# Kernel tuning notes

Measured on AMD Instinct MI355X. Metric: run time of the kernel, lower is better.

The kernel has to match this reference:

```python
import jax, jax.numpy as jnp
import numpy as np

N_HEADS = 4
NEG_SLOPE = 0.2  # DGL GATConv default leaky_relu slope


def setup_inputs() -> dict:
    key = jax.random.key(0)
    ks = jax.random.split(key, 12)
    N, E = 50000, 800000
    in_dim, time_dim, out_dim = 128, 128, 128
    d_head = out_dim // N_HEADS
    in_total = in_dim + time_dim
    h = jax.random.normal(ks[0], (N, in_dim), jnp.float32)
    time_tensor = jax.random.uniform(ks[1], (E,), jnp.float32)
    src = jax.random.randint(ks[2], (E,), 0, N, jnp.int32)
    dst = jax.random.randint(ks[3], (E,), 0, N, jnp.int32)
    # TimeEncoding: Linear(1, time_dim) with xavier weight, zero bias
    w_t = jax.random.normal(ks[4], (time_dim, 1), jnp.float32) * (6.0 / (1 + time_dim)) ** 0.5
    b_t = jnp.zeros((time_dim,), jnp.float32)
    # GATConv params
    W_fc = jax.random.normal(ks[5], (N_HEADS * d_head, in_total), jnp.float32) * (2.0 / in_total) ** 0.5
    attn_l = jax.random.normal(ks[6], (N_HEADS, d_head), jnp.float32) * 0.1
    attn_r = jax.random.normal(ks[7], (N_HEADS, d_head), jnp.float32) * 0.1
    W_res = jax.random.normal(ks[8], (N_HEADS * d_head, in_total), jnp.float32) * (2.0 / in_total) ** 0.5
    bias = jnp.zeros((N_HEADS * d_head,), jnp.float32)
    return {"h": h, "time_tensor": time_tensor, "src": src, "dst": dst,
            "num_nodes": N, "w_t": w_t, "b_t": b_t, "W_fc": W_fc,
            "attn_l": attn_l, "attn_r": attn_r, "W_res": W_res, "bias": bias}


def reference(h, time_tensor, src, dst, num_nodes, w_t, b_t, W_fc, attn_l, attn_r, W_res, bias):
    N = num_nodes
    E = src.shape[0]
    # Time encoding: cos(W t + b), per edge -> [E, time_dim]
    time_emb = jnp.cos(time_tensor[:, None] * w_t[:, 0][None, :] + b_t[None, :])
    # Mailbox mean of concat([src h, time_emb]) per dst node.
    # mean(concat) == concat(mean, mean), so sum the two halves separately.
    ones = jnp.ones((E,), h.dtype)
    deg = jax.ops.segment_sum(ones, dst, num_segments=N)  # [N]
    sum_h = jax.ops.segment_sum(h[src], dst, num_segments=N)       # [N, in_dim]
    sum_t = jax.ops.segment_sum(time_emb, dst, num_segments=N)     # [N, time_dim]
    inv_deg = 1.0 / jnp.maximum(deg, 1.0)
    h_time = jnp.concatenate([sum_h, sum_t], axis=1) * inv_deg[:, None]  # [N, in+time]
    # GATConv (eval mode, no dropout)
    d_head = W_fc.shape[0] // N_HEADS
    feat = (h_time @ W_fc.T).reshape(N, N_HEADS, d_head)  # [N,H,D]
    el = jnp.sum(feat * attn_l[None], axis=-1)  # [N,H]
    er = jnp.sum(feat * attn_r[None], axis=-1)  # [N,H]
    e = el[src] + er[dst]                        # [E,H]
    e = jnp.where(e > 0, e, NEG_SLOPE * e)
    # edge softmax over incoming edges of each dst node
    m = jax.ops.segment_max(e, dst, num_segments=N)  # [N,H]
    m = jnp.where(jnp.isfinite(m), m, 0.0)
    ex = jnp.exp(e - m[dst])
    denom = jax.ops.segment_sum(ex, dst, num_segments=N)
    a = ex / jnp.maximum(denom[dst], 1e-9)           # [E,H]
    rst = jax.ops.segment_sum(a[:, :, None] * feat[src], dst, num_segments=N)  # [N,H,D]
    res = (h_time @ W_res.T).reshape(N, N_HEADS, d_head)
    out = rst + res + bias.reshape(1, N_HEADS, d_head)
    out = jax.nn.elu(out)
    return out.reshape(N, -1)  # [N, out_dim]
```

## Files before the change

kernel.cpp:

```cpp
#include <hip/hip_runtime.h>
#include <math.h>

#define NH 4
#define NEG_SLOPE 0.2f
#define BKT_SHIFT 8
#define EPB 4096
#define CBLK 8192
#define INV2PI 0.15915494309189535f
#define LOG2E  1.4426950408889634f

typedef __attribute__((ext_vector_type(8))) short bf16x8;
typedef __attribute__((ext_vector_type(4))) float f32x4;
typedef __attribute__((ext_vector_type(2))) float f32x2;

__device__ __forceinline__ float blo(unsigned u) { return __uint_as_float(u << 16); }
__device__ __forceinline__ float bhi(unsigned u) { return __uint_as_float(u & 0xFFFF0000u); }
__device__ __forceinline__ f32x2 mk2(float a, float b) { f32x2 r; r.x = a; r.y = b; return r; }
__device__ __forceinline__ f32x2 unpk(unsigned u) { return mk2(blo(u), bhi(u)); }
__device__ __forceinline__ unsigned short rne(float f) {
    unsigned u = __float_as_uint(f);
    u += 0x7FFFu + ((u >> 16) & 1u);
    return (unsigned short)(u >> 16);
}
__device__ __forceinline__ unsigned pack2(float a, float b) {
    return (unsigned)rne(a) | ((unsigned)rne(b) << 16);
}

__global__ __launch_bounds__(256) void k_prep(
    const float* __restrict__ h, unsigned* __restrict__ hbu, int n_pairs,
    const float* __restrict__ Wfc, const float* __restrict__ Wres,
    unsigned* __restrict__ wcat,
    const float* __restrict__ w_t, const float* __restrict__ b_t,
    float2* __restrict__ w_s, float2* __restrict__ b_s,
    const int* __restrict__ dst, int* __restrict__ bkt_cnt, int E, int NB, int EB) {
    __shared__ int cnt[256];
    int tid = threadIdx.x;
    int t = blockIdx.x * blockDim.x + tid;
    if (t < n_pairs) {
        float2 v = ((const float2*)h)[t];
        hbu[t] = pack2(v.x, v.y);
    }
    if (t < 32768) {
        int col = t >> 7, kk = t & 127;
        const float* srcp = (col < 128) ? (Wfc + (size_t)col * 256)
                                        : (Wres + (size_t)(col - 128) * 256);
        float2 v = ((const float2*)srcp)[kk];
        int s  = col >> 6, ct = (col >> 4) & 3, r = col & 15;
        int ks = kk >> 4,  q  = (kk >> 2) & 3,  d = kk & 3;
        int w2i = ((s * 32 + ks * 4 + ct) << 8) + ((q * 16 + r) << 2) + d;
        wcat[w2i] = pack2(v.x, v.y);
    }
    if (t < 64) {
        float2 wv = ((const float2*)w_t)[t];
        float2 bv = ((const float2*)b_t)[t];
        w_s[t] = make_float2(wv.x * INV2PI, wv.y * INV2PI);
        b_s[t] = make_float2(bv.x * INV2PI, bv.y * INV2PI);
    }
    if (blockIdx.x < (unsigned)EB) {
        cnt[tid] = 0;
        __syncthreads();
        int q0 = (blockIdx.x * CBLK) >> 2;
#pragma unroll
        for (int k = 0; k < CBLK / 1024; k++) {
            int qi = q0 + k * 256 + tid;
            int base = qi * 4;
            if (base + 3 < E) {
                int4 dd = ((const int4*)dst)[qi];
                atomicAdd(&cnt[dd.x >> BKT_SHIFT], 1);
                atomicAdd(&cnt[dd.y >> BKT_SHIFT], 1);
                atomicAdd(&cnt[dd.z >> BKT_SHIFT], 1);
                atomicAdd(&cnt[dd.w >> BKT_SHIFT], 1);
            } else {
                for (int e = base; e < E; e++) atomicAdd(&cnt[dst[e] >> BKT_SHIFT], 1);
            }
        }
        __syncthreads();
        if (tid < NB) {
            int c = cnt[tid];
            if (c) atomicAdd(bkt_cnt + tid, c);
        }
    }
}

__global__ __launch_bounds__(256) void k_bktscan(
    const int* __restrict__ bkt_cnt, int* __restrict__ bkt_start,
    int* __restrict__ bkt_cursor, int* __restrict__ row_start,
    int NB, int E, int N) {
    __shared__ int wsum[4];
    int tid = threadIdx.x, lane = tid & 63, wid = tid >> 6;
    int v = (tid < NB) ? bkt_cnt[tid] : 0;
    int x = v;
#pragma unroll
    for (int off = 1; off < 64; off <<= 1) {
        int y = __shfl_up(x, off, 64);
        if (lane >= off) x += y;
    }
    if (lane == 63) wsum[wid] = x;
    __syncthreads();
    if (tid == 0) {
        int s = 0;
#pragma unroll
        for (int k = 0; k < 4; k++) { int tk = wsum[k]; wsum[k] = s; s += tk; }
    }
    __syncthreads();
    int excl = wsum[wid] + x - v;
    if (tid < NB) { bkt_start[tid] = excl; bkt_cursor[tid] = excl; }
    if (tid == 0) { bkt_start[NB] = E; row_start[N] = E; }
}

__global__ __launch_bounds__(256) void k_binscatter(
    const int* __restrict__ src, const int* __restrict__ dst,
    const float* __restrict__ tt, int* __restrict__ bkt_cursor,
    uint2* __restrict__ staged, int E, int NB) {
    __shared__ int cnt[1024];
    __shared__ int basep[1024];
    int e0 = blockIdx.x * EPB;
    int tid = threadIdx.x;
    for (int b = tid; b < NB; b += 256) cnt[b] = 0;
    __syncthreads();
#pragma unroll
    for (int k = 0; k < EPB / 256; k++) {
        int e = e0 + k * 256 + tid;
        if (e < E) atomicAdd(&cnt[dst[e] >> BKT_SHIFT], 1);
    }
    __syncthreads();
    for (int b = tid; b < NB; b += 256) {
        int c = cnt[b];
        basep[b] = (c > 0) ? atomicAdd(bkt_cursor + b, c) : 0;
        cnt[b] = 0;
    }
    __syncthreads();
#pragma unroll
    for (int k = 0; k < EPB / 256; k++) {
        int e = e0 + k * 256 + tid;
        if (e < E) {
            int d = dst[e];
            int b = d >> BKT_SHIFT;
            int r = atomicAdd(&cnt[b], 1);
            unsigned tq = min((unsigned)(tt[e] * 32768.0f), 32767u);
            staged[basep[b] + r] =
                make_uint2(((unsigned)src[e] << 15) | tq, (unsigned)(d & 255));
        }
    }
}

__global__ __launch_bounds__(256) void k_binsort(
    const uint2* __restrict__ staged, const int* __restrict__ bkt_start,
    int* __restrict__ row_start, unsigned* __restrict__ est, int N) {
    __shared__ int cnt[256];
    __shared__ int cur[256];
    __shared__ int wsum[4];
    __shared__ uint2 sst[8192];
    int b = blockIdx.x;
    int n0 = b << BKT_SHIFT;
    int tid = threadIdx.x;
    cnt[tid] = 0;
    __syncthreads();
    int s0 = bkt_start[b], s1 = bkt_start[b + 1];
    int run = s1 - s0;
    for (int p = tid; p < run; p += 256) {
        uint2 v = staged[s0 + p];
        if (p < 8192) sst[p] = v;
        atomicAdd(&cnt[v.y], 1);
    }
    __syncthreads();
    int lane = tid & 63, wid = tid >> 6;
    int v = cnt[tid];
    int x = v;
#pragma unroll
    for (int off = 1; off < 64; off <<= 1) {
        int y = __shfl_up(x, off, 64);
        if (lane >= off) x += y;
    }
    if (lane == 63) wsum[wid] = x;
    __syncthreads();
    if (tid == 0) {
        int s = 0;
#pragma unroll
        for (int k = 0; k < 4; k++) { int tk = wsum[k]; wsum[k] = s; s += tk; }
    }
    __syncthreads();
    int excl = s0 + wsum[wid] + x - v;
    cur[tid] = excl;
    if (n0 + tid < N) row_start[n0 + tid] = excl;
    __syncthreads();
    for (int p = tid; p < run; p += 256) {
        uint2 vv = (p < 8192) ? sst[p] : staged[s0 + p];
        int pos = atomicAdd(&cur[vv.y], 1);
        est[pos] = vv.x;
    }
}

__device__ __forceinline__ void agg_edge(unsigned u, const char* __restrict__ hb,
                                         int i, const f32x2* wv, const f32x2* bv,
                                         f32x2* aH, f32x2* aT) {
    unsigned off = (u >> 15) << 8;
    float t = (float)(u & 0x7FFFu) * (1.0f / 32768.0f) + (0.5f / 32768.0f);
    uint4 hv = *(const uint4*)(hb + off + i * 16);
    aH[0] += unpk(hv.x);
    aH[1] += unpk(hv.y);
    aH[2] += unpk(hv.z);
    aH[3] += unpk(hv.w);
    f32x2 t2 = mk2(t, t);
    f32x2 a0 = t2 * wv[0] + bv[0];
    f32x2 a1 = t2 * wv[1] + bv[1];
    f32x2 a2 = t2 * wv[2] + bv[2];
    f32x2 a3 = t2 * wv[3] + bv[3];
    aT[0] += mk2(__builtin_amdgcn_cosf(a0.x), __builtin_amdgcn_cosf(a0.y));
    aT[1] += mk2(__builtin_amdgcn_cosf(a1.x), __builtin_amdgcn_cosf(a1.y));
    aT[2] += mk2(__builtin_amdgcn_cosf(a2.x), __builtin_amdgcn_cosf(a2.y));
    aT[3] += mk2(__builtin_amdgcn_cosf(a3.x), __builtin_amdgcn_cosf(a3.y));
}

__device__ __forceinline__ void attn_edge(unsigned u, const char* __restrict__ fb,
                                          int i, int hd, const char* __restrict__ elb,
                                          float erh, f32x2* acc, float& den) {
    unsigned off = (u >> 15) << 8;
    float elh = *(const float*)(elb + (off >> 4) + (hd << 2));
    uint4 fv = *(const uint4*)(fb + off + i * 16);
    float w = elh + erh; w = w > 0.f ? w : NEG_SLOPE * w;
    float ex = __builtin_amdgcn_exp2f(w);
    f32x2 ex2 = mk2(ex, ex);
    acc[0] = ex2 * unpk(fv.x) + acc[0];
    acc[1] = ex2 * unpk(fv.y) + acc[1];
    acc[2] = ex2 * unpk(fv.z) + acc[2];
    acc[3] = ex2 * unpk(fv.w) + acc[3];
    den += ex;
}

__global__ __launch_bounds__(256) void k_agg(
    const unsigned* __restrict__ hbu, const unsigned* __restrict__ est,
    const int* __restrict__ row_start,
    const float2* __restrict__ w_s, const float2* __restrict__ b_s,
    unsigned* __restrict__ htu, int N) {
    int n = blockIdx.x * 4 + (threadIdx.x >> 6);
    if (n >= N) return;
    int lane = threadIdx.x & 63;
    int g = lane >> 4, i = lane & 15;
    int rs = row_start[n], re = row_start[n + 1];
    const char* hb = (const char*)hbu;
    const f32x2* wp = (const f32x2*)w_s;
    const f32x2* bp = (const f32x2*)b_s;
    f32x2 wv[4], bv[4];
#pragma unroll
    for (int k = 0; k < 4; k++) { wv[k] = wp[4 * i + k]; bv[k] = bp[4 * i + k]; }
    f32x2 aH[4] = {}, aT[4] = {};
    int nb = (re - rs) >> 4;
    int e = rs + g;
    for (int j = 0; j < nb; j++, e += 16) {
        unsigned u0 = est[e];
        unsigned u1 = est[e + 4];
        unsigned u2 = est[e + 8];
        unsigned u3 = est[e + 12];
        agg_edge(u0, hb, i, wv, bv, aH, aT);
        agg_edge(u1, hb, i, wv, bv, aH, aT);
        agg_edge(u2, hb, i, wv, bv, aH, aT);
        agg_edge(u3, hb, i, wv, bv, aH, aT);
    }
    for (; e < re; e += 4)
        agg_edge(est[e], hb, i, wv, bv, aH, aT);
#pragma unroll
    for (int off = 16; off <= 32; off <<= 1) {
#pragma unroll
        for (int k = 0; k < 4; k++) {
            aH[k].x += __shfl_xor(aH[k].x, off, 64);
            aH[k].y += __shfl_xor(aH[k].y, off, 64);
            aT[k].x += __shfl_xor(aT[k].x, off, 64);
            aT[k].y += __shfl_xor(aT[k].y, off, 64);
        }
    }
    if (g == 0) {
        int deg = re - rs;
        float idg = (deg > 0) ? 1.0f / (float)deg : 1.0f;
        uint4* ht4 = (uint4*)htu;
        uint4 oh, ot;
        oh.x = pack2(aH[0].x * idg, aH[0].y * idg);
        oh.y = pack2(aH[1].x * idg, aH[1].y * idg);
        oh.z = pack2(aH[2].x * idg, aH[2].y * idg);
        oh.w = pack2(aH[3].x * idg, aH[3].y * idg);
        ot.x = pack2(aT[0].x * idg, aT[0].y * idg);
        ot.y = pack2(aT[1].x * idg, aT[1].y * idg);
        ot.z = pack2(aT[2].x * idg, aT[2].y * idg);
        ot.w = pack2(aT[3].x * idg, aT[3].y * idg);
        ht4[(size_t)n * 32 + i]      = oh;
        ht4[(size_t)n * 32 + 16 + i] = ot;
    }
}

__global__ __launch_bounds__(256) void k_gemm(
    const unsigned short* __restrict__ ht, const unsigned* __restrict__ wcat,
    unsigned short* __restrict__ feat, float* __restrict__ res_out, int N) {
    __shared__ __align__(16) unsigned short As[64 * 264];
    int tid = threadIdx.x;
    int row0 = blockIdx.x * 64;
    const uint4* src4 = (const uint4*)ht;
    for (int idx = tid; idx < 64 * 32; idx += 256) {
        int rl = idx >> 5, c16 = idx & 31;
        int gr = row0 + rl; if (gr >= N) gr = N - 1;
        uint4 v = src4[(size_t)gr * 32 + c16];
        *(uint4*)(As + rl * 264 + c16 * 8) = v;
    }
    __syncthreads();
    int wave = tid >> 6, lane = tid & 63;
    int r = lane & 15, q = lane >> 4;
    int colbase = wave * 64;
    const bf16x8* bbase = (const bf16x8*)wcat + (size_t)wave * 2048 + lane;
    const unsigned short* abase = As + r * 264 + q * 8;
    f32x4 acc[4][4] = {};
#pragma unroll
    for (int ks = 0; ks < 8; ks++) {
        bf16x8 a[4], b[4];
#pragma unroll
        for (int rt = 0; rt < 4; rt++)
            a[rt] = *(const bf16x8*)(abase + rt * (16 * 264) + ks * 32);
#pragma unroll
        for (int ct = 0; ct < 4; ct++)
            b[ct] = bbase[(ks * 4 + ct) * 64];
#pragma unroll
        for (int rt = 0; rt < 4; rt++)
#pragma unroll
            for (int ct = 0; ct < 4; ct++)
                acc[rt][ct] = __builtin_amdgcn_mfma_f32_16x16x32_bf16(a[rt], b[ct], acc[rt][ct], 0, 0, 0);
    }
    bool featw = (colbase < 128);
#pragma unroll
    for (int rt = 0; rt < 4; rt++) {
        int rb = row0 + rt * 16 + q * 4;
#pragma unroll
        for (int ct = 0; ct < 4; ct++) {
            int col = colbase + ct * 16 + r;
#pragma unroll
            for (int reg = 0; reg < 4; reg++) {
                int row = rb + reg;
                if (row >= N) continue;
                float v = acc[rt][ct][reg];
                if (featw) feat[(size_t)row * 128 + col] = rne(v);
                else       res_out[(size_t)row * 128 + (col - 128)] = v;
            }
        }
    }
}

__global__ void k_el_er(const unsigned* __restrict__ featu,
                        const float* __restrict__ attn_l, const float* __restrict__ attn_r,
                        float* __restrict__ el, float* __restrict__ er, int NH4) {
    int t = blockIdx.x * blockDim.x + threadIdx.x;
    if (t >= NH4) return;
    int n = t >> 2, hd = t & 3;
    const unsigned* f = featu + (size_t)n * 64 + hd * 16;
    const float2* al = (const float2*)(attn_l + hd * 32);
    const float2* ar = (const float2*)(attn_r + hd * 32);
    float sl = 0.f, sr = 0.f;
#pragma unroll
    for (int i = 0; i < 16; i++) {
        unsigned u = f[i];
        float f0 = blo(u), f1 = bhi(u);
        float2 a = al[i], b = ar[i];
        sl = fmaf(f0, a.x, fmaf(f1, a.y, sl));
        sr = fmaf(f0, b.x, fmaf(f1, b.y, sr));
    }
    el[t] = sl * LOG2E;
    er[t] = sr * LOG2E;
}

__global__ __launch_bounds__(256) void k_attn(
    const unsigned* __restrict__ est, const int* __restrict__ row_start,
    const float* __restrict__ el, const float* __restrict__ er,
    const unsigned* __restrict__ featu, const float* __restrict__ bias,
    float* __restrict__ out, int N) {
    int n = blockIdx.x * 4 + (threadIdx.x >> 6);
    if (n >= N) return;
    int lane = threadIdx.x & 63;
    int g = lane >> 4, i = lane & 15;
    int hd = i >> 2;
    int rs = row_start[n], re = row_start[n + 1];
    float erh = er[(size_t)n * 4 + hd];
    const char* fb = (const char*)featu;
    const char* elb = (const char*)el;
    f32x2 acc[4] = {};
    float den = 0.f;
    int nb = (re - rs) >> 4;
    int e = rs + g;
    for (int j = 0; j < nb; j++, e += 16) {
        unsigned u0 = est[e];
        unsigned u1 = est[e + 4];
        unsigned u2 = est[e + 8];
        unsigned u3 = est[e + 12];
        attn_edge(u0, fb, i, hd, elb, erh, acc, den);
        attn_edge(u1, fb, i, hd, elb, erh, acc, den);
        attn_edge(u2, fb, i, hd, elb, erh, acc, den);
        attn_edge(u3, fb, i, hd, elb, erh, acc, den);
    }
    for (; e < re; e += 4)
        attn_edge(est[e], fb, i, hd, elb, erh, acc, den);
#pragma unroll
    for (int off = 16; off <= 32; off <<= 1) {
#pragma unroll
        for (int k = 0; k < 4; k++) {
            acc[k].x += __shfl_xor(acc[k].x, off, 64);
            acc[k].y += __shfl_xor(acc[k].y, off, 64);
        }
        den += __shfl_xor(den, off, 64);
    }
    if (g == 0) {
        float id = 1.0f / fmaxf(den, 1e-9f);
        float* op = out + (size_t)n * 128 + i * 8;
        const float* bp = bias + i * 8;
        float4 o0 = ((const float4*)op)[0], o1 = ((const float4*)op)[1];
        float4 b0 = ((const float4*)bp)[0], b1 = ((const float4*)bp)[1];
        float4 r0, r1;
        r0.x = fmaf(acc[0].x, id, o0.x + b0.x);
        r0.y = fmaf(acc[0].y, id, o0.y + b0.y);
        r0.z = fmaf(acc[1].x, id, o0.z + b0.z);
        r0.w = fmaf(acc[1].y, id, o0.w + b0.w);
        r1.x = fmaf(acc[2].x, id, o1.x + b1.x);
        r1.y = fmaf(acc[2].y, id, o1.y + b1.y);
        r1.z = fmaf(acc[3].x, id, o1.z + b1.z);
        r1.w = fmaf(acc[3].y, id, o1.w + b1.w);
        r0.x = r0.x > 0.f ? r0.x : (__expf(r0.x) - 1.0f);
        r0.y = r0.y > 0.f ? r0.y : (__expf(r0.y) - 1.0f);
        r0.z = r0.z > 0.f ? r0.z : (__expf(r0.z) - 1.0f);
        r0.w = r0.w > 0.f ? r0.w : (__expf(r0.w) - 1.0f);
        r1.x = r1.x > 0.f ? r1.x : (__expf(r1.x) - 1.0f);
        r1.y = r1.y > 0.f ? r1.y : (__expf(r1.y) - 1.0f);
        r1.z = r1.z > 0.f ? r1.z : (__expf(r1.z) - 1.0f);
        r1.w = r1.w > 0.f ? r1.w : (__expf(r1.w) - 1.0f);
        ((float4*)op)[0] = r0;
        ((float4*)op)[1] = r1;
    }
}

extern "C" void kernel_launch(void* const* d_in, const int* in_sizes, int n_in,
                              void* d_out, int out_size, void* d_ws, size_t ws_size,
                              hipStream_t stream) {
    const float* h     = (const float*)d_in[0];
    const float* tt    = (const float*)d_in[1];
    const int*   src   = (const int*)d_in[2];
    const int*   dst   = (const int*)d_in[3];
    const float* w_t   = (const float*)d_in[5];
    const float* b_t   = (const float*)d_in[6];
    const float* W_fc  = (const float*)d_in[7];
    const float* al    = (const float*)d_in[8];
    const float* ar    = (const float*)d_in[9];
    const float* W_res = (const float*)d_in[10];
    const float* bias  = (const float*)d_in[11];

    int N = in_sizes[0] / 128;
    int E = in_sizes[1];
    int NB = (N + 255) >> BKT_SHIFT;
    int EB = (E + CBLK - 1) / CBLK;

    char* ws = (char*)d_ws;
    size_t off = 0;
    auto alloc = [&](size_t bytes) { void* p = ws + off; off = (off + bytes + 15) & ~(size_t)15; return p; };
    unsigned* htu     = (unsigned*)alloc((size_t)N * 128 * 4);
    unsigned* hbu     = (unsigned*)alloc((size_t)N * 64 * 4);
    unsigned* featu   = (unsigned*)alloc((size_t)N * 64 * 4);
    unsigned* wcat    = (unsigned*)alloc(32768 * 4);
    float2*   w_s     = (float2*)alloc(64 * 8);
    float2*   b_s     = (float2*)alloc(64 * 8);
    float*    el      = (float*)alloc((size_t)N * NH * 4);
    float*    er      = (float*)alloc((size_t)N * NH * 4);
    int*      row_st  = (int*)alloc((size_t)(N + 1) * 4);
    int*      bkt_cur = (int*)alloc((size_t)NB * 4);
    int*      bkt_cnt = (int*)alloc((size_t)NB * 4);
    int*      bkt_sta = (int*)alloc((size_t)(NB + 1) * 4);
    unsigned* est     = (unsigned*)alloc((size_t)E * 4);
    uint2*    staged  = (uint2*)featu;

    hipMemsetAsync(bkt_cnt, 0, (size_t)NB * 4, stream);

    int prep_n = N * 64;
    hipLaunchKernelGGL(k_prep, dim3((prep_n + 255) / 256), dim3(256), 0, stream,
                       h, hbu, prep_n, W_fc, W_res, wcat, w_t, b_t, w_s, b_s,
                       dst, bkt_cnt, E, NB, EB);
    hipLaunchKernelGGL(k_bktscan, dim3(1), dim3(256), 0, stream,
                       bkt_cnt, bkt_sta, bkt_cur, row_st, NB, E, N);
    hipLaunchKernelGGL(k_binscatter, dim3((E + EPB - 1) / EPB), dim3(256), 0, stream,
                       src, dst, tt, bkt_cur, staged, E, NB);
    hipLaunchKernelGGL(k_binsort, dim3(NB), dim3(256), 0, stream,
                       staged, bkt_sta, row_st, est, N);
    hipLaunchKernelGGL(k_agg, dim3((N + 3) / 4), dim3(256), 0, stream,
                       hbu, est, row_st, w_s, b_s, htu, N);
    hipLaunchKernelGGL(k_gemm, dim3((N + 63) / 64), dim3(256), 0, stream,
                       (const unsigned short*)htu, wcat,
                       (unsigned short*)featu, (float*)d_out, N);
    hipLaunchKernelGGL(k_el_er, dim3((N * NH + 255) / 256), dim3(256), 0, stream,
                       featu, al, ar, el, er, N * NH);
    hipLaunchKernelGGL(k_attn, dim3((N + 3) / 4), dim3(256), 0, stream,
                       est, row_st, el, er, featu, bias, (float*)d_out, N);
}
```

Baseline: 249.0 us.

## Use precomputed cosine table for time encoding and persistent grid-stride agg/attn kernels

Replaces per-edge cosine evaluation in the aggregation kernel with a lookup into a 4096x128 cosine table built in k_prep, with the quantized time index truncated to 12 bits. Makes k_agg and k_attn persistent grid-stride kernels capped at 2048 blocks. Removes the shared-memory staging buffer in k_binsort so it reads staged entries from global memory twice. The table trades transcendental work for extra memory traffic and coarser time quantization, and the persistent loop may hurt load balance.

```diff
diff --git a/kernel.cpp b/kernel.cpp
--- a/kernel.cpp
+++ b/kernel.cpp
@@ -6,6 +6,7 @@
 #define BKT_SHIFT 8
 #define EPB 4096
 #define CBLK 8192
+#define TBLK 2048
 #define INV2PI 0.15915494309189535f
 #define LOG2E  1.4426950408889634f
 
@@ -31,7 +32,7 @@
     const float* __restrict__ Wfc, const float* __restrict__ Wres,
     unsigned* __restrict__ wcat,
     const float* __restrict__ w_t, const float* __restrict__ b_t,
-    float2* __restrict__ w_s, float2* __restrict__ b_s,
+    float* __restrict__ tbl,
     const int* __restrict__ dst, int* __restrict__ bkt_cnt, int E, int NB, int EB) {
     __shared__ int cnt[256];
     int tid = threadIdx.x;
@@ -49,12 +50,6 @@
         int ks = kk >> 4,  q  = (kk >> 2) & 3,  d = kk & 3;
         int w2i = ((s * 32 + ks * 4 + ct) << 8) + ((q * 16 + r) << 2) + d;
         wcat[w2i] = pack2(v.x, v.y);
-    }
-    if (t < 64) {
-        float2 wv = ((const float2*)w_t)[t];
-        float2 bv = ((const float2*)b_t)[t];
-        w_s[t] = make_float2(wv.x * INV2PI, wv.y * INV2PI);
-        b_s[t] = make_float2(bv.x * INV2PI, bv.y * INV2PI);
     }
     if (blockIdx.x < (unsigned)EB) {
         cnt[tid] = 0;
@@ -80,6 +75,15 @@
             if (c) atomicAdd(bkt_cnt + tid, c);
         }
     }
+    int tb = blockIdx.x - EB;
+    if (tb >= 0 && tb < TBLK) {
+        int idx = tb * 256 + tid;
+        int j = idx >> 7, d = idx & 127;
+        float wv = w_t[d] * INV2PI;
+        float bv = b_t[d] * INV2PI;
+        float tv = ((float)j + 0.5f) * (1.0f / 4096.0f);
+        tbl[idx] = __builtin_amdgcn_cosf(fmaf(tv, wv, bv));
+    }
 }
 
 __global__ __launch_bounds__(256) void k_bktscan(
@@ -150,19 +154,14 @@
     __shared__ int cnt[256];
     __shared__ int cur[256];
     __shared__ int wsum[4];
-    __shared__ uint2 sst[8192];
     int b = blockIdx.x;
     int n0 = b << BKT_SHIFT;
     int tid = threadIdx.x;
     cnt[tid] = 0;
     __syncthreads();
     int s0 = bkt_start[b], s1 = bkt_start[b + 1];
-    int run = s1 - s0;
-    for (int p = tid; p < run; p += 256) {
-        uint2 v = staged[s0 + p];
-        if (p < 8192) sst[p] = v;
-        atomicAdd(&cnt[v.y], 1);
-    }
+    for (int p = s0 + tid; p < s1; p += 256)
+        atomicAdd(&cnt[staged[p].y], 1);
     __syncthreads();
     int lane = tid & 63, wid = tid >> 6;
     int v = cnt[tid];
@@ -184,32 +183,29 @@
     cur[tid] = excl;
     if (n0 + tid < N) row_start[n0 + tid] = excl;
     __syncthreads();
-    for (int p = tid; p < run; p += 256) {
-        uint2 vv = (p < 8192) ? sst[p] : staged[s0 + p];
+    for (int p = s0 + tid; p < s1; p += 256) {
+        uint2 vv = staged[p];
         int pos = atomicAdd(&cur[vv.y], 1);
         est[pos] = vv.x;
     }
 }
 
 __device__ __forceinline__ void agg_edge(unsigned u, const char* __restrict__ hb,
-                                         int i, const f32x2* wv, const f32x2* bv,
+                                         const char* __restrict__ tb, int i,
                                          f32x2* aH, f32x2* aT) {
-    unsigned off = (u >> 15) << 8;
-    float t = (float)(u & 0x7FFFu) * (1.0f / 32768.0f) + (0.5f / 32768.0f);
-    uint4 hv = *(const uint4*)(hb + off + i * 16);
+    unsigned hoff = (u >> 15) << 8;
+    unsigned toff = (u & 0x7FF8u) << 6;
+    uint4 hv = *(const uint4*)(hb + hoff + i * 16);
+    const f32x4* cp = (const f32x4*)(tb + toff + i * 32);
+    f32x4 c0 = cp[0], c1 = cp[1];
     aH[0] += unpk(hv.x);
     aH[1] += unpk(hv.y);
     aH[2] += unpk(hv.z);
     aH[3] += unpk(hv.w);
-    f32x2 t2 = mk2(t, t);
-    f32x2 a0 = t2 * wv[0] + bv[0];
-    f32x2 a1 = t2 * wv[1] + bv[1];
-    f32x2 a2 = t2 * wv[2] + bv[2];
-    f32x2 a3 = t2 * wv[3] + bv[3];
-    aT[0] += mk2(__builtin_amdgcn_cosf(a0.x), __builtin_amdgcn_cosf(a0.y));
-    aT[1] += mk2(__builtin_amdgcn_cosf(a1.x), __builtin_amdgcn_cosf(a1.y));
-    aT[2] += mk2(__builtin_amdgcn_cosf(a2.x), __builtin_amdgcn_cosf(a2.y));
-    aT[3] += mk2(__builtin_amdgcn_cosf(a3.x), __builtin_amdgcn_cosf(a3.y));
+    aT[0] += mk2(c0.x, c0.y);
+    aT[1] += mk2(c0.z, c0.w);
+    aT[2] += mk2(c1.x, c1.y);
+    aT[3] += mk2(c1.z, c1.w);
 }
 
 __device__ __forceinline__ void attn_edge(unsigned u, const char* __restrict__ fb,
@@ -229,61 +225,58 @@
 }
 
 __global__ __launch_bounds__(256) void k_agg(
-    const unsigned* __restrict__ hbu, const unsigned* __restrict__ est,
-    const int* __restrict__ row_start,
-    const float2* __restrict__ w_s, const float2* __restrict__ b_s,
+    const unsigned* __restrict__ hbu, const float* __restrict__ tbl,
+    const unsigned* __restrict__ est, const int* __restrict__ row_start,
     unsigned* __restrict__ htu, int N) {
-    int n = blockIdx.x * 4 + (threadIdx.x >> 6);
-    if (n >= N) return;
     int lane = threadIdx.x & 63;
     int g = lane >> 4, i = lane & 15;
-    int rs = row_start[n], re = row_start[n + 1];
+    int wid = blockIdx.x * 4 + (threadIdx.x >> 6);
+    int nw = gridDim.x * 4;
     const char* hb = (const char*)hbu;
-    const f32x2* wp = (const f32x2*)w_s;
-    const f32x2* bp = (const f32x2*)b_s;
-    f32x2 wv[4], bv[4];
-#pragma unroll
-    for (int k = 0; k < 4; k++) { wv[k] = wp[4 * i + k]; bv[k] = bp[4 * i + k]; }
-    f32x2 aH[4] = {}, aT[4] = {};
-    int nb = (re - rs) >> 4;
-    int e = rs + g;
-    for (int j = 0; j < nb; j++, e += 16) {
-        unsigned u0 = est[e];
-        unsigned u1 = est[e + 4];
-        unsigned u2 = est[e + 8];
-        unsigned u3 = est[e + 12];
-        agg_edge(u0, hb, i, wv, bv, aH, aT);
-        agg_edge(u1, hb, i, wv, bv, aH, aT);
-        agg_edge(u2, hb, i, wv, bv, aH, aT);
-        agg_edge(u3, hb, i, wv, bv, aH, aT);
-    }
-    for (; e < re; e += 4)
-        agg_edge(est[e], hb, i, wv, bv, aH, aT);
-#pragma unroll
-    for (int off = 16; off <= 32; off <<= 1) {
-#pragma unroll
-        for (int k = 0; k < 4; k++) {
-            aH[k].x += __shfl_xor(aH[k].x, off, 64);
-            aH[k].y += __shfl_xor(aH[k].y, off, 64);
-            aT[k].x += __shfl_xor(aT[k].x, off, 64);
-            aT[k].y += __shfl_xor(aT[k].y, off, 64);
-        }
-    }
-    if (g == 0) {
-        int deg = re - rs;
-        float idg = (deg > 0) ? 1.0f / (float)deg : 1.0f;
-        uint4* ht4 = (uint4*)htu;
-        uint4 oh, ot;
-        oh.x = pack2(aH[0].x * idg, aH[0].y * idg);
-        oh.y = pack2(aH[1].x * idg, aH[1].y * idg);
-        oh.z = pack2(aH[2].x * idg, aH[2].y * idg);
-        oh.w = pack2(aH[3].x * idg, aH[3].y * idg);
-        ot.x = pack2(aT[0].x * idg, aT[0].y * idg);
-        ot.y = pack2(aT[1].x * idg, aT[1].y * idg);
-        ot.z = pack2(aT[2].x * idg, aT[2].y * idg);
-        ot.w = pack2(aT[3].x * idg, aT[3].y * idg);
-        ht4[(size_t)n * 32 + i]      = oh;
-        ht4[(size_t)n * 32 + 16 + i] = ot;
+    const char* tb = (const char*)tbl;
+    for (int n = wid; n < N; n += nw) {
+        int rs = row_start[n], re = row_start[n + 1];
+        f32x2 aH[4] = {}, aT[4] = {};
+        int nb = (re - rs) >> 4;
+        int e = rs + g;
+        for (int j = 0; j < nb; j++, e += 16) {
+            unsigned u0 = est[e];
+            unsigned u1 = est[e + 4];
+            unsigned u2 = est[e + 8];
+            unsigned u3 = est[e + 12];
+            agg_edge(u0, hb, tb, i, aH, aT);
+            agg_edge(u1, hb, tb, i, aH, aT);
+            agg_edge(u2, hb, tb, i, aH, aT);
+            agg_edge(u3, hb, tb, i, aH, aT);
+        }
+        for (; e < re; e += 4)
+            agg_edge(est[e], hb, tb, i, aH, aT);
+#pragma unroll
+        for (int off = 16; off <= 32; off <<= 1) {
+#pragma unroll
+            for (int k = 0; k < 4; k++) {
+                aH[k].x += __shfl_xor(aH[k].x, off, 64);
+                aH[k].y += __shfl_xor(aH[k].y, off, 64);
+                aT[k].x += __shfl_xor(aT[k].x, off, 64);
+                aT[k].y += __shfl_xor(aT[k].y, off, 64);
+            }
+        }
+        if (g == 0) {
+            int deg = re - rs;
+            float idg = (deg > 0) ? 1.0f / (float)deg : 1.0f;
+            uint4* ht4 = (uint4*)htu;
+            uint4 oh, ot;
+            oh.x = pack2(aH[0].x * idg, aH[0].y * idg);
+            oh.y = pack2(aH[1].x * idg, aH[1].y * idg);
+            oh.z = pack2(aH[2].x * idg, aH[2].y * idg);
+            oh.w = pack2(aH[3].x * idg, aH[3].y * idg);
+            ot.x = pack2(aT[0].x * idg, aT[0].y * idg);
+            ot.y = pack2(aT[1].x * idg, aT[1].y * idg);
+            ot.z = pack2(aT[2].x * idg, aT[2].y * idg);
+            ot.w = pack2(aT[3].x * idg, aT[3].y * idg);
+            ht4[(size_t)n * 32 + i]      = oh;
+            ht4[(size_t)n * 32 + 16 + i] = ot;
+        }
     }
 }
 
@@ -368,65 +361,67 @@
     const float* __restrict__ el, const float* __restrict__ er,
     const unsigned* __restrict__ featu, const float* __restrict__ bias,
     float* __restrict__ out, int N) {
-    int n = blockIdx.x * 4 + (threadIdx.x >> 6);
-    if (n >= N) return;
     int lane = threadIdx.x & 63;
     int g = lane >> 4, i = lane & 15;
     int hd = i >> 2;
-    int rs = row_start[n], re = row_start[n + 1];
-    float erh = er[(size_t)n * 4 + hd];
+    int wid = blockIdx.x * 4 + (threadIdx.x >> 6);
+    int nw = gridDim.x * 4;
     const char* fb = (const char*)featu;
     const char* elb = (const char*)el;
-    f32x2 acc[4] = {};
-    float den = 0.f;
-    int nb = (re - rs) >> 4;
-    int e = rs + g;
-    for (int j = 0; j < nb; j++, e += 16) {
-        unsigned u0 = est[e];
-        unsigned u1 = est[e + 4];
-        unsigned u2 = est[e + 8];
-        unsigned u3 = est[e + 12];
-        attn_edge(u0, fb, i, hd, elb, erh, acc, den);
-        attn_edge(u1, fb, i, hd, elb, erh, acc, den);
-        attn_edge(u2, fb, i, hd, elb, erh, acc, den);
-        attn_edge(u3, fb, i, hd, elb, erh, acc, den);
-    }
-    for (; e < re; e += 4)
-        attn_edge(est[e], fb, i, hd, elb, erh, acc, den);
-#pragma unroll
-    for (int off = 16; off <= 32; off <<= 1) {
-#pragma unroll
-        for (int k = 0; k < 4; k++) {
-            acc[k].x += __shfl_xor(acc[k].x, off, 64);
-            acc[k].y += __shfl_xor(acc[k].y, off, 64);
-        }
-        den += __shfl_xor(den, off, 64);
-    }
-    if (g == 0) {
-        float id = 1.0f / fmaxf(den, 1e-9f);
-        float* op = out + (size_t)n * 128 + i * 8;
-        const float* bp = bias + i * 8;
-        float4 o0 = ((const float4*)op)[0], o1 = ((const float4*)op)[1];
-        float4 b0 = ((const float4*)bp)[0], b1 = ((const float4*)bp)[1];
-        float4 r0, r1;
-        r0.x = fmaf(acc[0].x, id, o0.x + b0.x);
-        r0.y = fmaf(acc[0].y, id, o0.y + b0.y);
-        r0.z = fmaf(acc[1].x, id, o0.z + b0.z);
-        r0.w = fmaf(acc[1].y, id, o0.w + b0.w);
-        r1.x = fmaf(acc[2].x, id, o1.x + b1.x);
-        r1.y = fmaf(acc[2].y, id, o1.y + b1.y);
-        r1.z = fmaf(acc[3].x, id, o1.z + b1.z);
-        r1.w = fmaf(acc[3].y, id, o1.w + b1.w);
-        r0.x = r0.x > 0.f ? r0.x : (__expf(r0.x) - 1.0f);
-        r0.y = r0.y > 0.f ? r0.y : (__expf(r0.y) - 1.0f);
-        r0.z = r0.z > 0.f ? r0.z : (__expf(r0.z) - 1.0f);
-        r0.w = r0.w > 0.f ? r0.w : (__expf(r0.w) - 1.0f);
-        r1.x = r1.x > 0.f ? r1.x : (__expf(r1.x) - 1.0f);
-        r1.y = r1.y > 0.f ? r1.y : (__expf(r1.y) - 1.0f);
-        r1.z = r1.z > 0.f ? r1.z : (__expf(r1.z) - 1.0f);
-        r1.w = r1.w > 0.f ? r1.w : (__expf(r1.w) - 1.0f);
-        ((float4*)op)[0] = r0;
-        ((float4*)op)[1] = r1;
+    for (int n = wid; n < N; n += nw) {
+        int rs = row_start[n], re = row_start[n + 1];
+        float erh = er[(size_t)n * 4 + hd];
+        f32x2 acc[4] = {};
+        float den = 0.f;
+        int nb = (re - rs) >> 4;
+        int e = rs + g;
+        for (int j = 0; j < nb; j++, e += 16) {
+            unsigned u0 = est[e];
+            unsigned u1 = est[e + 4];
+            unsigned u2 = est[e + 8];
+            unsigned u3 = est[e + 12];
+            attn_edge(u0, fb, i, hd, elb, erh, acc, den);
+            attn_edge(u1, fb, i, hd, elb, erh, acc, den);
+            attn_edge(u2, fb, i, hd, elb, erh, acc, den);
+            attn_edge(u3, fb, i, hd, elb, erh, acc, den);
+        }
+        for (; e < re; e += 4)
+            attn_edge(est[e], fb, i, hd, elb, erh, acc, den);
+#pragma unroll
+        for (int off = 16; off <= 32; off <<= 1) {
+#pragma unroll
+            for (int k = 0; k < 4; k++) {
+                acc[k].x += __shfl_xor(acc[k].x, off, 64);
+                acc[k].y += __shfl_xor(acc[k].y, off, 64);
+            }
+            den += __shfl_xor(den, off, 64);
+        }
+        if (g == 0) {
+            float id = 1.0f / fmaxf(den, 1e-9f);
+            float* op = out + (size_t)n * 128 + i * 8;
+            const float* bp = bias + i * 8;
+            float4 o0 = ((const float4*)op)[0], o1 = ((const float4*)op)[1];
+            float4 b0 = ((const float4*)bp)[0], b1 = ((const float4*)bp)[1];
+            float4 r0, r1;
+            r0.x = fmaf(acc[0].x, id, o0.x + b0.x);
+            r0.y = fmaf(acc[0].y, id, o0.y + b0.y);
+            r0.z = fmaf(acc[1].x, id, o0.z + b0.z);
+            r0.w = fmaf(acc[1].y, id, o0.w + b0.w);
+            r1.x = fmaf(acc[2].x, id, o1.x + b1.x);
+            r1.y = fmaf(acc[2].y, id, o1.y + b1.y);
+            r1.z = fmaf(acc[3].x, id, o1.z + b1.z);
+            r1.w = fmaf(acc[3].y, id, o1.w + b1.w);
+            r0.x = r0.x > 0.f ? r0.x : (__expf(r0.x) - 1.0f);
+            r0.y = r0.y > 0.f ? r0.y : (__expf(r0.y) - 1.0f);
+            r0.z = r0.z > 0.f ? r0.z : (__expf(r0.z) - 1.0f);
+            r0.w = r0.w > 0.f ? r0.w : (__expf(r0.w) - 1.0f);
+            r1.x = r1.x > 0.f ? r1.x : (__expf(r1.x) - 1.0f);
+            r1.y = r1.y > 0.f ? r1.y : (__expf(r1.y) - 1.0f);
+            r1.z = r1.z > 0.f ? r1.z : (__expf(r1.z) - 1.0f);
+            r1.w = r1.w > 0.f ? r1.w : (__expf(r1.w) - 1.0f);
+            ((float4*)op)[0] = r0;
+            ((float4*)op)[1] = r1;
+        }
     }
 }
 
@@ -457,8 +452,7 @@
     unsigned* hbu     = (unsigned*)alloc((size_t)N * 64 * 4);
     unsigned* featu   = (unsigned*)alloc((size_t)N * 64 * 4);
     unsigned* wcat    = (unsigned*)alloc(32768 * 4);
-    float2*   w_s     = (float2*)alloc(64 * 8);
-    float2*   b_s     = (float2*)alloc(64 * 8);
+    float*    tbl     = (float*)alloc((size_t)4096 * 128 * 4);
     float*    el      = (float*)alloc((size_t)N * NH * 4);
     float*    er      = (float*)alloc((size_t)N * NH * 4);
     int*      row_st  = (int*)alloc((size_t)(N + 1) * 4);
@@ -472,7 +466,7 @@
 
     int prep_n = N * 64;
     hipLaunchKernelGGL(k_prep, dim3((prep_n + 255) / 256), dim3(256), 0, stream,
-                       h, hbu, prep_n, W_fc, W_res, wcat, w_t, b_t, w_s, b_s,
+                       h, hbu, prep_n, W_fc, W_res, wcat, w_t, b_t, tbl,
                        dst, bkt_cnt, E, NB, EB);
     hipLaunchKernelGGL(k_bktscan, dim3(1), dim3(256), 0, stream,
                        bkt_cnt, bkt_sta, bkt_cur, row_st, NB, E, N);
@@ -480,13 +474,14 @@
                        src, dst, tt, bkt_cur, staged, E, NB);
     hipLaunchKernelGGL(k_binsort, dim3(NB), dim3(256), 0, stream,
                        staged, bkt_sta, row_st, est, N);
-    hipLaunchKernelGGL(k_agg, dim3((N + 3) / 4), dim3(256), 0, stream,
-                       hbu, est, row_st, w_s, b_s, htu, N);
+    int npersist = min((N + 3) / 4, 2048);
+    hipLaunchKernelGGL(k_agg, dim3(npersist), dim3(256), 0, stream,
+                       hbu, tbl, est, row_st, htu, N);
     hipLaunchKernelGGL(k_gemm, dim3((N + 63) / 64), dim3(256), 0, stream,
                        (const unsigned short*)htu, wcat,
                        (unsigned short*)featu, (float*)d_out, N);
     hipLaunchKernelGGL(k_el_er, dim3((N * NH + 255) / 256), dim3(256), 0, stream,
                        featu, al, ar, el, er, N * NH);
-    hipLaunchKernelGGL(k_attn, dim3((N + 3) / 4), dim3(256), 0, stream,
+    hipLaunchKernelGGL(k_attn, dim3(npersist), dim3(256), 0, stream,
                        est, row_st, el, er, featu, bias, (float*)d_out, N);
 }
```

New measurement: 275.3 us. +10.6%, slower.
